# Optimization experiments

Measured on AMD Instinct MI355X. Metric: run time of the kernel, lower is better.

The kernel has to match this reference:

```python
import jax, jax.numpy as jnp
import numpy as np

N, E, IN, HID, OUT, HEADS = 50000, 800000, 256, 256, 128, 4
HC = HID // HEADS  # 64
EPS = 1e-5


def layer_norm(x, g, b):
    mu = x.mean(-1, keepdims=True)
    var = ((x - mu) ** 2).mean(-1, keepdims=True)
    return (x - mu) * jax.lax.rsqrt(var + EPS) * g + b


def gat_conv(x, W, a_s, a_d, bias, src, dst, heads, C, concat):
    # PyG GATConv (eval mode): linear -> per-edge LeakyReLU attention ->
    # segment softmax over destination -> scatter-sum aggregation -> bias
    n = x.shape[0]
    xw = (x @ W).reshape(n, heads, C)                     # [N,H,C]
    al_s = jnp.einsum('nhc,hc->nh', xw, a_s)              # [N,H]
    al_d = jnp.einsum('nhc,hc->nh', xw, a_d)
    e = jax.nn.leaky_relu(al_s[src] + al_d[dst], 0.2)     # [Etot,H]
    m = jax.ops.segment_max(e, dst, num_segments=n)
    ex = jnp.exp(e - m[dst])
    denom = jax.ops.segment_sum(ex, dst, num_segments=n)
    alpha = ex / denom[dst]                               # [Etot,H]
    out = jax.ops.segment_sum(xw[src] * alpha[:, :, None], dst, num_segments=n)
    out = out.reshape(n, heads * C) if concat else out.mean(axis=1)
    return out + bias


def setup_inputs() -> dict:
    key = jax.random.key(0)
    ks = jax.random.split(key, 20)
    s = 0.05
    return {
        'x': jax.random.normal(ks[0], (N, IN), jnp.float32),
        'edge_index': jax.random.randint(ks[1], (2, E), 0, N, jnp.int64),
        'Wp': jax.random.normal(ks[2], (IN, HID), jnp.float32) * s,
        'bp': jnp.zeros((HID,), jnp.float32),
        'W0': jax.random.normal(ks[3], (HID, HEADS * HC), jnp.float32) * s,
        'as0': jax.random.normal(ks[4], (HEADS, HC), jnp.float32) * s,
        'ad0': jax.random.normal(ks[5], (HEADS, HC), jnp.float32) * s,
        'b0': jnp.zeros((HID,), jnp.float32),
        'W1': jax.random.normal(ks[6], (HID, OUT), jnp.float32) * s,
        'as1': jax.random.normal(ks[7], (1, OUT), jnp.float32) * s,
        'ad1': jax.random.normal(ks[8], (1, OUT), jnp.float32) * s,
        'b1': jnp.zeros((OUT,), jnp.float32),
        'g0': jnp.ones((HID,), jnp.float32),
        'be0': jnp.zeros((HID,), jnp.float32),
        'g1': jnp.ones((OUT,), jnp.float32),
        'be1': jnp.zeros((OUT,), jnp.float32),
        'Wo': jax.random.normal(ks[9], (OUT, OUT), jnp.float32) * s,
        'bo': jnp.zeros((OUT,), jnp.float32),
    }


def reference(x, edge_index, Wp, bp, W0, as0, ad0, b0, W1, as1, ad1, b1,
              g0, be0, g1, be1, Wo, bo):
    n = x.shape[0]
    # add self loops (PyG GATConv default)
    ar = jnp.arange(n, dtype=edge_index.dtype)
    src = jnp.concatenate([edge_index[0], ar])
    dst = jnp.concatenate([edge_index[1], ar])

    h = jax.nn.relu(x @ Wp + bp)
    # layer 0: multi-head, concat, LN + residual + relu
    h1 = gat_conv(h, W0, as0, ad0, b0, src, dst, HEADS, HC, True)
    h1 = layer_norm(h1, g0, be0)
    h1 = jax.nn.relu(h1 + h)
    # layer 1: single head, no concat, LN (no residual: shape check still passes
    # only when identity is not None; here identity is None for last layer)
    h2 = gat_conv(h1, W1, as1, ad1, b1, src, dst, 1, OUT, False)
    h2 = layer_norm(h2, g1, be1)
    out = h2 @ Wo + bo
    out = out / jnp.maximum(jnp.linalg.norm(out, axis=-1, keepdims=True), 1e-12)
    return out
```

## Files before the change

kernel.cpp:

```cpp
#include <hip/hip_runtime.h>
#include <hip/hip_bf16.h>

typedef __bf16 bf16x8 __attribute__((ext_vector_type(8)));
typedef __bf16 bf16x4 __attribute__((ext_vector_type(4)));
typedef __bf16 bf16x2 __attribute__((ext_vector_type(2)));
typedef float f32x4 __attribute__((ext_vector_type(4)));

__device__ __forceinline__ float getf(const void* p, size_t i, int isf32){
  return isf32 ? ((const float*)p)[i]
               : __bfloat162float(((const __hip_bfloat16*)p)[i]);
}
__device__ __forceinline__ int getedge(const void* p, long long idx, int is64, int n){
  long long v = is64 ? ((const long long*)p)[idx] : (long long)((const int*)p)[idx];
  v = v < 0 ? 0 : (v >= n ? (long long)(n - 1) : v);
  return (int)v;
}

__device__ __forceinline__ float bfly_sum(float v){
#pragma unroll
  for (int m = 32; m > 0; m >>= 1) v += __shfl_xor(v, m, 64);
  return v;
}

__global__ __launch_bounds__(256) void detect_kernel(const void* x, const void* ei,
                                                     int* flags){
  __shared__ int cnt_sane, cnt_odd;
  int t = threadIdx.x;
  if (t == 0){ cnt_sane = 0; cnt_odd = 0; }
  __syncthreads();
  int sane = 0;
  for (int i = t; i < 4096; i += 256){
    float v = __bfloat162float(((const __hip_bfloat16*)x)[i]);
    if (fabsf(v) < 16.f) sane++;
  }
  atomicAdd(&cnt_sane, sane);
  int odd = 0;
  for (int i = t; i < 512; i += 256){
    if (((const int*)ei)[2 * i + 1] != 0) odd++;
  }
  atomicAdd(&cnt_odd, odd);
  __syncthreads();
  if (t == 0){
    flags[0] = (cnt_sane < 3900) ? 1 : 0;
    flags[1] = (cnt_odd == 0) ? 1 : 0;
  }
}

__global__ __launch_bounds__(256) void count_kernel(const void* __restrict__ ei, long long E,
                                                    int n, const int* __restrict__ flags,
                                                    int* __restrict__ cnt){
  int i = blockIdx.x * blockDim.x + threadIdx.x;
  if (i < E){
    int d = getedge(ei, E + i, flags[1], n);
    atomicAdd(&cnt[d], 1);
  }
}

__global__ __launch_bounds__(1024) void scan_kernel(const int* __restrict__ cnt, int* __restrict__ off,
                                                    int* __restrict__ pos, int n){
  __shared__ int wsum[16];
  __shared__ int carry_s;
  int tid = threadIdx.x, lane = tid & 63, wv = tid >> 6;
  if (tid == 0) carry_s = 0;
  __syncthreads();
  for (int base = 0; base < n; base += 4096){
    int i0 = base + tid * 4;
    int v0 = 0, v1 = 0, v2 = 0, v3 = 0;
    if (i0 + 3 < n){
      int4 q = *(const int4*)(cnt + i0);
      v0 = q.x; v1 = q.y; v2 = q.z; v3 = q.w;
    } else {
      if (i0 < n)     v0 = cnt[i0];
      if (i0 + 1 < n) v1 = cnt[i0 + 1];
      if (i0 + 2 < n) v2 = cnt[i0 + 2];
      if (i0 + 3 < n) v3 = cnt[i0 + 3];
    }
    int s4 = v0 + v1 + v2 + v3;
    int s = s4;
#pragma unroll
    for (int o = 1; o < 64; o <<= 1){ int t = __shfl_up(s, o, 64); if (lane >= o) s += t; }
    if (lane == 63) wsum[wv] = s;
    __syncthreads();
    int wo = 0;
    for (int w = 0; w < wv; w++) wo += wsum[w];
    int carry = carry_s;
    int e0 = carry + wo + s - s4;
    if (i0 + 3 < n){
      int4 o4; o4.x = e0; o4.y = e0 + v0; o4.z = e0 + v0 + v1; o4.w = e0 + v0 + v1 + v2;
      *(int4*)(off + i0) = o4;
      *(int4*)(pos + i0) = o4;
    } else {
      if (i0 < n)     { off[i0] = e0;               pos[i0] = e0; }
      if (i0 + 1 < n) { off[i0+1] = e0+v0;          pos[i0+1] = e0+v0; }
      if (i0 + 2 < n) { off[i0+2] = e0+v0+v1;       pos[i0+2] = e0+v0+v1; }
      if (i0 + 3 < n) { off[i0+3] = e0+v0+v1+v2;    pos[i0+3] = e0+v0+v1+v2; }
    }
    __syncthreads();
    if (tid == 0){
      int tot = 0;
      for (int w = 0; w < 16; w++) tot += wsum[w];
      carry_s = carry + tot;
    }
    __syncthreads();
  }
  if (tid == 0) off[n] = carry_s;
}

__global__ __launch_bounds__(256) void fill_kernel(const void* __restrict__ ei, long long E,
                                                   int n, const int* __restrict__ flags,
                                                   int* __restrict__ pos, int* __restrict__ bsrc){
  int i = blockIdx.x * blockDim.x + threadIdx.x;
  if (i < E){
    int d = getedge(ei, E + i, flags[1], n);
    int s = getedge(ei, i, flags[1], n);
    int p = atomicAdd(&pos[d], 1);
    bsrc[p] = s;
  }
}

__global__ __launch_bounds__(256) void transpose_all_kernel(
    const void* __restrict__ Wp, const void* __restrict__ W0,
    const void* __restrict__ W1, const void* __restrict__ Wo,
    const int* __restrict__ flags,
    __hip_bfloat16* __restrict__ btp, __hip_bfloat16* __restrict__ bt0,
    __hip_bfloat16* __restrict__ bt1, __hip_bfloat16* __restrict__ bto)
{
  int f0 = flags[0];
  int o = blockIdx.x * 256 + threadIdx.x;
  const void* W; __hip_bfloat16* B; int K, N, loc;
  if (o < 65536)       { W = Wp; B = btp; K = 256; N = 256; loc = o; }
  else if (o < 131072) { W = W0; B = bt0; K = 256; N = 256; loc = o - 65536; }
  else if (o < 163840) { W = W1; B = bt1; K = 256; N = 128; loc = o - 131072; }
  else if (o < 180224) { W = Wo; B = bto; K = 128; N = 128; loc = o - 163840; }
  else return;
  int nn = loc / K, kk = loc - nn * K;
  B[loc] = __float2bfloat16(getf(W, (size_t)kk * N + nn, f0));
}

__device__ __forceinline__ bf16x8 pk8(f32x4 u, f32x4 w){
  bf16x8 r;
  r[0] = (__bf16)u.x; r[1] = (__bf16)u.y; r[2] = (__bf16)u.z; r[3] = (__bf16)u.w;
  r[4] = (__bf16)w.x; r[5] = (__bf16)w.y; r[6] = (__bf16)w.z; r[7] = (__bf16)w.w;
  return r;
}

template<int AMODE, bool OUTF, bool OUTB, bool RELU, bool BIAS, bool NORM, int ALMODE>
__global__ __launch_bounds__(256) void gemm_direct_kernel(
    const void* __restrict__ A, const __hip_bfloat16* __restrict__ Bt,
    const void* __restrict__ bias, const void* __restrict__ a_s, const void* __restrict__ a_d,
    const int* __restrict__ flags,
    float* __restrict__ Cf, __hip_bfloat16* __restrict__ Cb,
    float* __restrict__ als, float* __restrict__ ald,
    int M, int N, int K)
{
  const int f0 = flags[0];
  const bool af32 = (AMODE == 1) && (f0 != 0);
  int t = threadIdx.x;
  int wave = t >> 6, lane = t & 63;
  int q = lane >> 4, mi = lane & 15;
  int bm = blockIdx.x * 128 + wave * 32;
  int bn = blockIdx.y * 128;

  int r0 = min(bm + mi, M - 1);
  int r1 = min(bm + 16 + mi, M - 1);

  f32x4 acc[2][8] = {};

  if (af32){
    const float* Af = (const float*)A;
    const float* p0 = Af + (size_t)r0 * K + q * 8;
    const float* p1 = Af + (size_t)r1 * K + q * 8;
#pragma unroll 2
    for (int k0 = 0; k0 < K; k0 += 32){
      f32x4 u0 = *(const f32x4*)(p0 + k0);
      f32x4 w0 = *(const f32x4*)(p0 + k0 + 4);
      f32x4 u1 = *(const f32x4*)(p1 + k0);
      f32x4 w1 = *(const f32x4*)(p1 + k0 + 4);
      bf16x8 a0 = pk8(u0, w0);
      bf16x8 a1 = pk8(u1, w1);
#pragma unroll
      for (int nt = 0; nt < 8; nt++){
        bf16x8 b = *(const bf16x8*)(Bt + (size_t)(bn + nt * 16 + mi) * K + k0 + q * 8);
        acc[0][nt] = __builtin_amdgcn_mfma_f32_16x16x32_bf16(a0, b, acc[0][nt], 0, 0, 0);
        acc[1][nt] = __builtin_amdgcn_mfma_f32_16x16x32_bf16(a1, b, acc[1][nt], 0, 0, 0);
      }
    }
  } else {
    const __hip_bfloat16* Ab = (const __hip_bfloat16*)A;
    const __hip_bfloat16* p0 = Ab + (size_t)r0 * K + q * 8;
    const __hip_bfloat16* p1 = Ab + (size_t)r1 * K + q * 8;
#pragma unroll 2
    for (int k0 = 0; k0 < K; k0 += 32){
      bf16x8 a0 = *(const bf16x8*)(p0 + k0);
      bf16x8 a1 = *(const bf16x8*)(p1 + k0);
#pragma unroll
      for (int nt = 0; nt < 8; nt++){
        bf16x8 b = *(const bf16x8*)(Bt + (size_t)(bn + nt * 16 + mi) * K + k0 + q * 8);
        acc[0][nt] = __builtin_amdgcn_mfma_f32_16x16x32_bf16(a0, b, acc[0][nt], 0, 0, 0);
        acc[1][nt] = __builtin_amdgcn_mfma_f32_16x16x32_bf16(a1, b, acc[1][nt], 0, 0, 0);
      }
    }
  }

  float bv[8], asv[8], adv[8];
  if (BIAS){
#pragma unroll
    for (int nt = 0; nt < 8; nt++) bv[nt] = getf(bias, bn + nt * 16 + mi, f0);
  }
  if (ALMODE != 0){
#pragma unroll
    for (int nt = 0; nt < 8; nt++){
      asv[nt] = getf(a_s, bn + nt * 16 + mi, f0);
      adv[nt] = getf(a_d, bn + nt * 16 + mi, f0);
    }
  }
#pragma unroll
  for (int mt = 0; mt < 2; mt++){
#pragma unroll
    for (int r = 0; r < 4; r++){
      int row = bm + mt * 16 + q * 4 + r;
      float vv[8];
#pragma unroll
      for (int nt = 0; nt < 8; nt++){
        float v = acc[mt][nt][r];
        if (BIAS) v += bv[nt];
        if (RELU) v = fmaxf(v, 0.f);
        vv[nt] = v;
      }
      if (NORM){
        float ss = 0.f;
#pragma unroll
        for (int nt = 0; nt < 8; nt++) ss += vv[nt] * vv[nt];
        ss += __shfl_xor(ss, 1, 64);
        ss += __shfl_xor(ss, 2, 64);
        ss += __shfl_xor(ss, 4, 64);
        ss += __shfl_xor(ss, 8, 64);
        float inv = 1.f / fmaxf(sqrtf(ss), 1e-12f);
#pragma unroll
        for (int nt = 0; nt < 8; nt++) vv[nt] *= inv;
      }
      if (ALMODE == 1){
        float ps0 = 0.f, pd0 = 0.f, ps1 = 0.f, pd1 = 0.f;
#pragma unroll
        for (int nt = 0; nt < 4; nt++){ ps0 += vv[nt] * asv[nt]; pd0 += vv[nt] * adv[nt]; }
#pragma unroll
        for (int nt = 4; nt < 8; nt++){ ps1 += vv[nt] * asv[nt]; pd1 += vv[nt] * adv[nt]; }
#pragma unroll
        for (int m = 1; m < 16; m <<= 1){
          ps0 += __shfl_xor(ps0, m, 64); pd0 += __shfl_xor(pd0, m, 64);
          ps1 += __shfl_xor(ps1, m, 64); pd1 += __shfl_xor(pd1, m, 64);
        }
        if ((lane & 15) == 0 && row < M){
          int h0 = blockIdx.y * 2;
          als[(size_t)row * 4 + h0]     = ps0; ald[(size_t)row * 4 + h0]     = pd0;
          als[(size_t)row * 4 + h0 + 1] = ps1; ald[(size_t)row * 4 + h0 + 1] = pd1;
        }
      } else if (ALMODE == 2){
        float ps = 0.f, pd = 0.f;
#pragma unroll
        for (int nt = 0; nt < 8; nt++){ ps += vv[nt] * asv[nt]; pd += vv[nt] * adv[nt]; }
#pragma unroll
        for (int m = 1; m < 16; m <<= 1){
          ps += __shfl_xor(ps, m, 64); pd += __shfl_xor(pd, m, 64);
        }
        if ((lane & 15) == 0 && row < M){ als[row] = ps; ald[row] = pd; }
      }
      if (row < M){
#pragma unroll
        for (int nt = 0; nt < 8; nt++){
          int col = bn + nt * 16 + mi;
          size_t idx = (size_t)row * N + col;
          if (OUTF) Cf[idx] = vv[nt];
          if (OUTB) Cb[idx] = __float2bfloat16(vv[nt]);
        }
      }
    }
  }
}

#define FMA4(U, W) do { \
  m0 += (W) * __uint_as_float((U).x << 16); \
  m1 += (W) * __uint_as_float((U).x & 0xffff0000u); \
  m2 += (W) * __uint_as_float((U).y << 16); \
  m3 += (W) * __uint_as_float((U).y & 0xffff0000u); \
} while (0)

__global__ __launch_bounds__(256) void gather0_kernel(
    const __hip_bfloat16* __restrict__ xw, const float* __restrict__ als, const float* __restrict__ ald,
    const int* __restrict__ bsrc, const int* __restrict__ off,
    const void* __restrict__ bias, const void* __restrict__ gamma,
    const void* __restrict__ beta, const int* __restrict__ flags,
    __hip_bfloat16* __restrict__ hbuf, int n)
{
  int f0 = flags[0];
  int t = threadIdx.x, wv = t >> 6, lane = t & 63;
  int i = blockIdx.x * 4 + wv;
  if (i >= n) return;
  int head = lane >> 4;
  int ch = lane * 4;
  int e0 = off[i], jend = off[i + 1];

  float m0 = 0.f, m1 = 0.f, m2 = 0.f, m3 = 0.f;

  float aldi = ald[(size_t)i * 4 + head];

  float se = als[(size_t)i * 4 + head] + aldi;
  se = (se > 0.f) ? se : 0.2f * se;
  float eself = __expf(se);
  {
    uint2 u = *(const uint2*)(xw + (size_t)i * 256 + ch);
    FMA4(u, eself);
  }
  float wacc = eself;

  int j = e0;
  for (; j + 3 < jend; j += 4){
    int s0 = bsrc[j], s1 = bsrc[j + 1], s2 = bsrc[j + 2], s3 = bsrc[j + 3];
    float l0 = als[(size_t)s0 * 4 + head] + aldi;
    float l1 = als[(size_t)s1 * 4 + head] + aldi;
    float l2 = als[(size_t)s2 * 4 + head] + aldi;
    float l3 = als[(size_t)s3 * 4 + head] + aldi;
    l0 = (l0 > 0.f) ? l0 : 0.2f * l0;
    l1 = (l1 > 0.f) ? l1 : 0.2f * l1;
    l2 = (l2 > 0.f) ? l2 : 0.2f * l2;
    l3 = (l3 > 0.f) ? l3 : 0.2f * l3;
    float w0 = __expf(l0), w1 = __expf(l1), w2 = __expf(l2), w3 = __expf(l3);
    uint2 U0 = *(const uint2*)(xw + (size_t)s0 * 256 + ch);
    uint2 U1 = *(const uint2*)(xw + (size_t)s1 * 256 + ch);
    uint2 U2 = *(const uint2*)(xw + (size_t)s2 * 256 + ch);
    uint2 U3 = *(const uint2*)(xw + (size_t)s3 * 256 + ch);
    wacc += w0 + w1 + w2 + w3;
    FMA4(U0, w0); FMA4(U1, w1); FMA4(U2, w2); FMA4(U3, w3);
  }
  for (; j < jend; j++){
    int s0 = bsrc[j];
    float l0 = als[(size_t)s0 * 4 + head] + aldi;
    l0 = (l0 > 0.f) ? l0 : 0.2f * l0;
    float w0 = __expf(l0);
    uint2 U0 = *(const uint2*)(xw + (size_t)s0 * 256 + ch);
    wacc += w0;
    FMA4(U0, w0);
  }

  float rl = 1.f / wacc;
  float v0 = m0 * rl + getf(bias, ch + 0, f0);
  float v1 = m1 * rl + getf(bias, ch + 1, f0);
  float v2 = m2 * rl + getf(bias, ch + 2, f0);
  float v3 = m3 * rl + getf(bias, ch + 3, f0);

  float mu = bfly_sum(v0 + v1 + v2 + v3) * (1.f / 256.f);
  float d0 = v0 - mu, d1 = v1 - mu, d2 = v2 - mu, d3 = v3 - mu;
  float var = bfly_sum(d0 * d0 + d1 * d1 + d2 * d2 + d3 * d3) * (1.f / 256.f);
  float rs = rsqrtf(var + 1e-5f);

  bf16x4 rb = *(const bf16x4*)(hbuf + (size_t)i * 256 + ch);
  float y0 = fmaxf(d0 * rs * getf(gamma, ch + 0, f0) + getf(beta, ch + 0, f0) + (float)rb[0], 0.f);
  float y1 = fmaxf(d1 * rs * getf(gamma, ch + 1, f0) + getf(beta, ch + 1, f0) + (float)rb[1], 0.f);
  float y2 = fmaxf(d2 * rs * getf(gamma, ch + 2, f0) + getf(beta, ch + 2, f0) + (float)rb[2], 0.f);
  float y3 = fmaxf(d3 * rs * getf(gamma, ch + 3, f0) + getf(beta, ch + 3, f0) + (float)rb[3], 0.f);

  bf16x4 o;
  o[0] = (__bf16)y0; o[1] = (__bf16)y1; o[2] = (__bf16)y2; o[3] = (__bf16)y3;
  *(bf16x4*)(hbuf + (size_t)i * 256 + ch) = o;
}

#define FMA2(U, W) do { \
  m0 += (W) * __uint_as_float((U) << 16); \
  m1 += (W) * __uint_as_float((U) & 0xffff0000u); \
} while (0)

__global__ __launch_bounds__(256) void gather1_kernel(
    const __hip_bfloat16* __restrict__ xw, const float* __restrict__ als, const float* __restrict__ ald,
    const int* __restrict__ bsrc, const int* __restrict__ off,
    const void* __restrict__ bias, const void* __restrict__ gamma,
    const void* __restrict__ beta, const int* __restrict__ flags,
    __hip_bfloat16* __restrict__ outb, int n)
{
  int f0 = flags[0];
  int t = threadIdx.x, wv = t >> 6, lane = t & 63;
  int i = blockIdx.x * 4 + wv;
  if (i >= n) return;
  int ch = lane * 2;
  int e0 = off[i], jend = off[i + 1];

  float m0 = 0.f, m1 = 0.f;

  float aldi = ald[i];
  float se = als[i] + aldi;
  se = (se > 0.f) ? se : 0.2f * se;
  float eself = __expf(se);
  {
    unsigned u = *(const unsigned*)(xw + (size_t)i * 128 + ch);
    FMA2(u, eself);
  }
  float wacc = eself;

  int j = e0;
  for (; j + 3 < jend; j += 4){
    int s0 = bsrc[j], s1 = bsrc[j + 1], s2 = bsrc[j + 2], s3 = bsrc[j + 3];
    float l0 = als[s0] + aldi, l1 = als[s1] + aldi, l2 = als[s2] + aldi, l3 = als[s3] + aldi;
    l0 = (l0 > 0.f) ? l0 : 0.2f * l0;
    l1 = (l1 > 0.f) ? l1 : 0.2f * l1;
    l2 = (l2 > 0.f) ? l2 : 0.2f * l2;
    l3 = (l3 > 0.f) ? l3 : 0.2f * l3;
    float w0 = __expf(l0), w1 = __expf(l1), w2 = __expf(l2), w3 = __expf(l3);
    unsigned U0 = *(const unsigned*)(xw + (size_t)s0 * 128 + ch);
    unsigned U1 = *(const unsigned*)(xw + (size_t)s1 * 128 + ch);
    unsigned U2 = *(const unsigned*)(xw + (size_t)s2 * 128 + ch);
    unsigned U3 = *(const unsigned*)(xw + (size_t)s3 * 128 + ch);
    wacc += w0 + w1 + w2 + w3;
    FMA2(U0, w0); FMA2(U1, w1); FMA2(U2, w2); FMA2(U3, w3);
  }
  for (; j < jend; j++){
    int s0 = bsrc[j];
    float l0 = als[s0] + aldi;
    l0 = (l0 > 0.f) ? l0 : 0.2f * l0;
    float w0 = __expf(l0);
    unsigned U0 = *(const unsigned*)(xw + (size_t)s0 * 128 + ch);
    wacc += w0;
    FMA2(U0, w0);
  }

  float rl = 1.f / wacc;
  float v0 = m0 * rl + getf(bias, ch + 0, f0);
  float v1 = m1 * rl + getf(bias, ch + 1, f0);

  float mu = bfly_sum(v0 + v1) * (1.f / 128.f);
  float d0 = v0 - mu, d1 = v1 - mu;
  float var = bfly_sum(d0 * d0 + d1 * d1) * (1.f / 128.f);
  float rs = rsqrtf(var + 1e-5f);

  float y0 = d0 * rs * getf(gamma, ch + 0, f0) + getf(beta, ch + 0, f0);
  float y1 = d1 * rs * getf(gamma, ch + 1, f0) + getf(beta, ch + 1, f0);

  bf16x2 o;
  o[0] = (__bf16)y0; o[1] = (__bf16)y1;
  *(bf16x2*)(outb + (size_t)i * 128 + ch) = o;
}

extern "C" void kernel_launch(void* const* d_in, const int* in_sizes, int n_in,
                              void* d_out, int out_size, void* d_ws, size_t ws_size,
                              hipStream_t stream)
{
  const void* x   = d_in[0];
  const void* ei  = d_in[1];
  const void* Wp  = d_in[2];
  const void* bp  = d_in[3];
  const void* W0  = d_in[4];
  const void* as0 = d_in[5];
  const void* ad0 = d_in[6];
  const void* b0  = d_in[7];
  const void* W1  = d_in[8];
  const void* as1 = d_in[9];
  const void* ad1 = d_in[10];
  const void* b1  = d_in[11];
  const void* g0  = d_in[12];
  const void* be0 = d_in[13];
  const void* g1  = d_in[14];
  const void* be1 = d_in[15];
  const void* Wo  = d_in[16];
  const void* bo  = d_in[17];
  float* outp = (float*)d_out;

  const int n = in_sizes[0] / 256;
  const int E = in_sizes[1] / 2;

  char* w = (char*)d_ws;
  size_t SZ = (size_t)n * 256 * sizeof(float);
  __hip_bfloat16* h_bf  = (__hip_bfloat16*)w;
  __hip_bfloat16* xw_bf = (__hip_bfloat16*)(w + SZ / 2);
  char* p = w + SZ;
  int* flags = (int*)p; p += 64;
  float* als0 = (float*)p; p += (size_t)n * 4 * sizeof(float);
  float* ald0 = (float*)p; p += (size_t)n * 4 * sizeof(float);
  float* als1 = (float*)p; p += (size_t)n * sizeof(float);
  float* ald1 = (float*)p; p += (size_t)n * sizeof(float);
  int* cnt  = (int*)p; p += (size_t)n * sizeof(int);
  int* offb = (int*)p; p += (size_t)(n + 4) * sizeof(int);
  int* pos  = (int*)p; p += (size_t)n * sizeof(int);
  int* bsrc = (int*)p; p += (size_t)E * sizeof(int);
  p = (char*)(((uintptr_t)p + 15) & ~(uintptr_t)15);
  __hip_bfloat16* bt_p = (__hip_bfloat16*)p; p += (size_t)256 * 256 * 2;
  __hip_bfloat16* bt_0 = (__hip_bfloat16*)p; p += (size_t)256 * 256 * 2;
  __hip_bfloat16* bt_1 = (__hip_bfloat16*)p; p += (size_t)128 * 256 * 2;
  __hip_bfloat16* bt_o = (__hip_bfloat16*)p; p += (size_t)128 * 128 * 2;

  detect_kernel<<<1, 256, 0, stream>>>(x, ei, flags);

  transpose_all_kernel<<<704, 256, 0, stream>>>(Wp, W0, W1, Wo, flags, bt_p, bt_0, bt_1, bt_o);

  hipMemsetAsync(cnt, 0, (size_t)n * sizeof(int), stream);
  count_kernel<<<(E + 255) / 256, 256, 0, stream>>>(ei, E, n, flags, cnt);
  scan_kernel<<<1, 1024, 0, stream>>>(cnt, offb, pos, n);
  fill_kernel<<<(E + 255) / 256, 256, 0, stream>>>(ei, E, n, flags, pos, bsrc);

  int gm = (n + 127) / 128;
  int gn4 = (n + 3) / 4;

  gemm_direct_kernel<1, false, true, true, true, false, 0><<<dim3(gm, 2), 256, 0, stream>>>(
      x, bt_p, bp, nullptr, nullptr, flags, nullptr, h_bf, nullptr, nullptr, n, 256, 256);
  gemm_direct_kernel<0, false, true, false, false, false, 1><<<dim3(gm, 2), 256, 0, stream>>>(
      h_bf, bt_0, nullptr, as0, ad0, flags, nullptr, xw_bf, als0, ald0, n, 256, 256);
  gather0_kernel<<<gn4, 256, 0, stream>>>(xw_bf, als0, ald0, bsrc, offb, b0, g0, be0,
                                          flags, h_bf, n);
  gemm_direct_kernel<0, false, true, false, false, false, 2><<<dim3(gm, 1), 256, 0, stream>>>(
      h_bf, bt_1, nullptr, as1, ad1, flags, nullptr, xw_bf, als1, ald1, n, 128, 256);
  gather1_kernel<<<gn4, 256, 0, stream>>>(xw_bf, als1, ald1, bsrc, offb, b1, g1, be1,
                                          flags, h_bf, n);
  gemm_direct_kernel<0, true, false, false, true, true, 0><<<dim3(gm, 1), 256, 0, stream>>>(
      h_bf, bt_o, bo, nullptr, nullptr, flags, outp, nullptr, nullptr, nullptr, n, 128, 128);
}
```

Before: 496.4 us.

## Sort nodes by degree and split each wave across two edge streams in gathers

Adds a degree histogram, scan and scatter that build a node order sorted by descending in-degree, so the waves in a block see similar amounts of work. Both gather kernels now split each 64-lane wave into two half-waves that process alternating edges with wider per-lane loads (8 or 4 bf16 channels). The half-wave partial sums are combined with a cross-lane shuffle before the layer norm. This costs three small extra kernels and a loss of node locality in the output writes.

New measurement: 821.7 us. +65.5%, slower.

```diff
diff --git a/kernel.cpp b/kernel.cpp
--- a/kernel.cpp
+++ b/kernel.cpp
@@ -5,6 +5,7 @@
 typedef __bf16 bf16x4 __attribute__((ext_vector_type(4)));
 typedef __bf16 bf16x2 __attribute__((ext_vector_type(2)));
 typedef float f32x4 __attribute__((ext_vector_type(4)));
+typedef unsigned u32x4 __attribute__((ext_vector_type(4)));
 
 __device__ __forceinline__ float getf(const void* p, size_t i, int isf32){
   return isf32 ? ((const float*)p)[i]
@@ -21,6 +22,9 @@
   for (int m = 32; m > 0; m >>= 1) v += __shfl_xor(v, m, 64);
   return v;
 }
+
+__device__ __forceinline__ float bf_lo(unsigned u){ return __uint_as_float(u << 16); }
+__device__ __forceinline__ float bf_hi(unsigned u){ return __uint_as_float(u & 0xffff0000u); }
 
 __global__ __launch_bounds__(256) void detect_kernel(const void* x, const void* ei,
                                                      int* flags){
@@ -118,6 +122,37 @@
   }
 }
 
+__global__ __launch_bounds__(256) void deghist_kernel(const int* __restrict__ cnt, int n,
+                                                      int* __restrict__ hist){
+  int i = blockIdx.x * 256 + threadIdx.x;
+  if (i < n){ int b = min(cnt[i], 255); atomicAdd(&hist[b], 1); }
+}
+
+__global__ __launch_bounds__(256) void degscan_kernel(const int* __restrict__ hist,
+                                                      int* __restrict__ binpos){
+  __shared__ int h[256];
+  int t = threadIdx.x;
+  h[t] = hist[t];
+  __syncthreads();
+  if (t == 0){
+    int acc = 0;
+    for (int b = 255; b >= 0; b--){ int c = h[b]; h[b] = acc; acc += c; }
+  }
+  __syncthreads();
+  binpos[t] = h[t];
+}
+
+__global__ __launch_bounds__(256) void degscatter_kernel(const int* __restrict__ cnt, int n,
+                                                         int* __restrict__ binpos,
+                                                         int* __restrict__ order){
+  int i = blockIdx.x * 256 + threadIdx.x;
+  if (i < n){
+    int b = min(cnt[i], 255);
+    int p = atomicAdd(&binpos[b], 1);
+    order[p] = i;
+  }
+}
+
 __global__ __launch_bounds__(256) void transpose_all_kernel(
     const void* __restrict__ Wp, const void* __restrict__ W0,
     const void* __restrict__ W1, const void* __restrict__ Wo,
@@ -278,44 +313,53 @@
   }
 }
 
-#define FMA4(U, W) do { \
-  m0 += (W) * __uint_as_float((U).x << 16); \
-  m1 += (W) * __uint_as_float((U).x & 0xffff0000u); \
-  m2 += (W) * __uint_as_float((U).y << 16); \
-  m3 += (W) * __uint_as_float((U).y & 0xffff0000u); \
+#define UFMA8(U, W) do { \
+  m0 += (W) * bf_lo((U).x); m1 += (W) * bf_hi((U).x); \
+  m2 += (W) * bf_lo((U).y); m3 += (W) * bf_hi((U).y); \
+  m4 += (W) * bf_lo((U).z); m5 += (W) * bf_hi((U).z); \
+  m6 += (W) * bf_lo((U).w); m7 += (W) * bf_hi((U).w); \
+} while (0)
+
+#define UFMA4(U, W) do { \
+  m0 += (W) * bf_lo((U).x); m1 += (W) * bf_hi((U).x); \
+  m2 += (W) * bf_lo((U).y); m3 += (W) * bf_hi((U).y); \
 } while (0)
 
 __global__ __launch_bounds__(256) void gather0_kernel(
     const __hip_bfloat16* __restrict__ xw, const float* __restrict__ als, const float* __restrict__ ald,
-    const int* __restrict__ bsrc, const int* __restrict__ off,
+    const int* __restrict__ bsrc, const int* __restrict__ off, const int* __restrict__ order,
     const void* __restrict__ bias, const void* __restrict__ gamma,
     const void* __restrict__ beta, const int* __restrict__ flags,
     __hip_bfloat16* __restrict__ hbuf, int n)
 {
   int f0 = flags[0];
   int t = threadIdx.x, wv = t >> 6, lane = t & 63;
-  int i = blockIdx.x * 4 + wv;
-  if (i >= n) return;
-  int head = lane >> 4;
-  int ch = lane * 4;
+  int idx = blockIdx.x * 4 + wv;
+  if (idx >= n) return;
+  int i = order[idx];
+  int es = lane >> 5;
+  int sl = lane & 31;
+  int ch = sl * 8;
+  int head = sl >> 3;
   int e0 = off[i], jend = off[i + 1];
 
-  float m0 = 0.f, m1 = 0.f, m2 = 0.f, m3 = 0.f;
-
+  float m0=0.f,m1=0.f,m2=0.f,m3=0.f,m4=0.f,m5=0.f,m6=0.f,m7=0.f;
   float aldi = ald[(size_t)i * 4 + head];
 
   float se = als[(size_t)i * 4 + head] + aldi;
   se = (se > 0.f) ? se : 0.2f * se;
   float eself = __expf(se);
-  {
-    uint2 u = *(const uint2*)(xw + (size_t)i * 256 + ch);
-    FMA4(u, eself);
-  }
-  float wacc = eself;
-
-  int j = e0;
-  for (; j + 3 < jend; j += 4){
-    int s0 = bsrc[j], s1 = bsrc[j + 1], s2 = bsrc[j + 2], s3 = bsrc[j + 3];
+  float wacc = 0.f;
+  if (es == 0){
+    uint4 u = *(const uint4*)(xw + (size_t)i * 256 + ch);
+    UFMA8(u, eself);
+    wacc = eself;
+  }
+
+  for (int j = e0 + es; j < jend; j += 8){
+    int j1 = j + 2, j2 = j + 4, j3 = j + 6;
+    int c1 = min(j1, jend - 1), c2 = min(j2, jend - 1), c3 = min(j3, jend - 1);
+    int s0 = bsrc[j], s1 = bsrc[c1], s2 = bsrc[c2], s3 = bsrc[c3];
     float l0 = als[(size_t)s0 * 4 + head] + aldi;
     float l1 = als[(size_t)s1 * 4 + head] + aldi;
     float l2 = als[(size_t)s2 * 4 + head] + aldi;
@@ -324,118 +368,130 @@
     l1 = (l1 > 0.f) ? l1 : 0.2f * l1;
     l2 = (l2 > 0.f) ? l2 : 0.2f * l2;
     l3 = (l3 > 0.f) ? l3 : 0.2f * l3;
-    float w0 = __expf(l0), w1 = __expf(l1), w2 = __expf(l2), w3 = __expf(l3);
-    uint2 U0 = *(const uint2*)(xw + (size_t)s0 * 256 + ch);
-    uint2 U1 = *(const uint2*)(xw + (size_t)s1 * 256 + ch);
-    uint2 U2 = *(const uint2*)(xw + (size_t)s2 * 256 + ch);
-    uint2 U3 = *(const uint2*)(xw + (size_t)s3 * 256 + ch);
+    float w0 = __expf(l0);
+    float w1 = (j1 < jend) ? __expf(l1) : 0.f;
+    float w2 = (j2 < jend) ? __expf(l2) : 0.f;
+    float w3 = (j3 < jend) ? __expf(l3) : 0.f;
+    uint4 U0 = *(const uint4*)(xw + (size_t)s0 * 256 + ch);
+    uint4 U1 = *(const uint4*)(xw + (size_t)s1 * 256 + ch);
+    uint4 U2 = *(const uint4*)(xw + (size_t)s2 * 256 + ch);
+    uint4 U3 = *(const uint4*)(xw + (size_t)s3 * 256 + ch);
     wacc += w0 + w1 + w2 + w3;
-    FMA4(U0, w0); FMA4(U1, w1); FMA4(U2, w2); FMA4(U3, w3);
-  }
-  for (; j < jend; j++){
-    int s0 = bsrc[j];
-    float l0 = als[(size_t)s0 * 4 + head] + aldi;
-    l0 = (l0 > 0.f) ? l0 : 0.2f * l0;
-    float w0 = __expf(l0);
-    uint2 U0 = *(const uint2*)(xw + (size_t)s0 * 256 + ch);
-    wacc += w0;
-    FMA4(U0, w0);
-  }
+    UFMA8(U0, w0); UFMA8(U1, w1); UFMA8(U2, w2); UFMA8(U3, w3);
+  }
+
+  m0 += __shfl_xor(m0, 32, 64); m1 += __shfl_xor(m1, 32, 64);
+  m2 += __shfl_xor(m2, 32, 64); m3 += __shfl_xor(m3, 32, 64);
+  m4 += __shfl_xor(m4, 32, 64); m5 += __shfl_xor(m5, 32, 64);
+  m6 += __shfl_xor(m6, 32, 64); m7 += __shfl_xor(m7, 32, 64);
+  wacc += __shfl_xor(wacc, 32, 64);
 
   float rl = 1.f / wacc;
   float v0 = m0 * rl + getf(bias, ch + 0, f0);
   float v1 = m1 * rl + getf(bias, ch + 1, f0);
   float v2 = m2 * rl + getf(bias, ch + 2, f0);
   float v3 = m3 * rl + getf(bias, ch + 3, f0);
-
-  float mu = bfly_sum(v0 + v1 + v2 + v3) * (1.f / 256.f);
-  float d0 = v0 - mu, d1 = v1 - mu, d2 = v2 - mu, d3 = v3 - mu;
-  float var = bfly_sum(d0 * d0 + d1 * d1 + d2 * d2 + d3 * d3) * (1.f / 256.f);
+  float v4 = m4 * rl + getf(bias, ch + 4, f0);
+  float v5 = m5 * rl + getf(bias, ch + 5, f0);
+  float v6 = m6 * rl + getf(bias, ch + 6, f0);
+  float v7 = m7 * rl + getf(bias, ch + 7, f0);
+
+  float mu = bfly_sum(v0+v1+v2+v3+v4+v5+v6+v7) * (1.f / 512.f);
+  float d0=v0-mu,d1=v1-mu,d2=v2-mu,d3=v3-mu,d4=v4-mu,d5=v5-mu,d6=v6-mu,d7=v7-mu;
+  float var = bfly_sum(d0*d0+d1*d1+d2*d2+d3*d3+d4*d4+d5*d5+d6*d6+d7*d7) * (1.f / 512.f);
   float rs = rsqrtf(var + 1e-5f);
 
-  bf16x4 rb = *(const bf16x4*)(hbuf + (size_t)i * 256 + ch);
-  float y0 = fmaxf(d0 * rs * getf(gamma, ch + 0, f0) + getf(beta, ch + 0, f0) + (float)rb[0], 0.f);
-  float y1 = fmaxf(d1 * rs * getf(gamma, ch + 1, f0) + getf(beta, ch + 1, f0) + (float)rb[1], 0.f);
-  float y2 = fmaxf(d2 * rs * getf(gamma, ch + 2, f0) + getf(beta, ch + 2, f0) + (float)rb[2], 0.f);
-  float y3 = fmaxf(d3 * rs * getf(gamma, ch + 3, f0) + getf(beta, ch + 3, f0) + (float)rb[3], 0.f);
-
-  bf16x4 o;
-  o[0] = (__bf16)y0; o[1] = (__bf16)y1; o[2] = (__bf16)y2; o[3] = (__bf16)y3;
-  *(bf16x4*)(hbuf + (size_t)i * 256 + ch) = o;
-}
-
-#define FMA2(U, W) do { \
-  m0 += (W) * __uint_as_float((U) << 16); \
-  m1 += (W) * __uint_as_float((U) & 0xffff0000u); \
-} while (0)
+  if (es == 0){
+    u32x4 rbu = __builtin_nontemporal_load((const u32x4*)(hbuf + (size_t)i * 256 + ch));
+    bf16x8 rb = __builtin_bit_cast(bf16x8, rbu);
+    bf16x8 o;
+    float y;
+    y = d0 * rs * getf(gamma, ch+0, f0) + getf(beta, ch+0, f0) + (float)rb[0]; o[0] = (__bf16)fmaxf(y, 0.f);
+    y = d1 * rs * getf(gamma, ch+1, f0) + getf(beta, ch+1, f0) + (float)rb[1]; o[1] = (__bf16)fmaxf(y, 0.f);
+    y = d2 * rs * getf(gamma, ch+2, f0) + getf(beta, ch+2, f0) + (float)rb[2]; o[2] = (__bf16)fmaxf(y, 0.f);
+    y = d3 * rs * getf(gamma, ch+3, f0) + getf(beta, ch+3, f0) + (float)rb[3]; o[3] = (__bf16)fmaxf(y, 0.f);
+    y = d4 * rs * getf(gamma, ch+4, f0) + getf(beta, ch+4, f0) + (float)rb[4]; o[4] = (__bf16)fmaxf(y, 0.f);
+    y = d5 * rs * getf(gamma, ch+5, f0) + getf(beta, ch+5, f0) + (float)rb[5]; o[5] = (__bf16)fmaxf(y, 0.f);
+    y = d6 * rs * getf(gamma, ch+6, f0) + getf(beta, ch+6, f0) + (float)rb[6]; o[6] = (__bf16)fmaxf(y, 0.f);
+    y = d7 * rs * getf(gamma, ch+7, f0) + getf(beta, ch+7, f0) + (float)rb[7]; o[7] = (__bf16)fmaxf(y, 0.f);
+    *(bf16x8*)(hbuf + (size_t)i * 256 + ch) = o;
+  }
+}
 
 __global__ __launch_bounds__(256) void gather1_kernel(
     const __hip_bfloat16* __restrict__ xw, const float* __restrict__ als, const float* __restrict__ ald,
-    const int* __restrict__ bsrc, const int* __restrict__ off,
+    const int* __restrict__ bsrc, const int* __restrict__ off, const int* __restrict__ order,
     const void* __restrict__ bias, const void* __restrict__ gamma,
     const void* __restrict__ beta, const int* __restrict__ flags,
     __hip_bfloat16* __restrict__ outb, int n)
 {
   int f0 = flags[0];
   int t = threadIdx.x, wv = t >> 6, lane = t & 63;
-  int i = blockIdx.x * 4 + wv;
-  if (i >= n) return;
-  int ch = lane * 2;
+  int idx = blockIdx.x * 4 + wv;
+  if (idx >= n) return;
+  int i = order[idx];
+  int es = lane >> 5;
+  int sl = lane & 31;
+  int ch = sl * 4;
   int e0 = off[i], jend = off[i + 1];
 
-  float m0 = 0.f, m1 = 0.f;
-
+  float m0=0.f,m1=0.f,m2=0.f,m3=0.f;
   float aldi = ald[i];
   float se = als[i] + aldi;
   se = (se > 0.f) ? se : 0.2f * se;
   float eself = __expf(se);
-  {
-    unsigned u = *(const unsigned*)(xw + (size_t)i * 128 + ch);
-    FMA2(u, eself);
-  }
-  float wacc = eself;
-
-  int j = e0;
-  for (; j + 3 < jend; j += 4){
-    int s0 = bsrc[j], s1 = bsrc[j + 1], s2 = bsrc[j + 2], s3 = bsrc[j + 3];
+  float wacc = 0.f;
+  if (es == 0){
+    uint2 u = *(const uint2*)(xw + (size_t)i * 128 + ch);
+    UFMA4(u, eself);
+    wacc = eself;
+  }
+
+  for (int j = e0 + es; j < jend; j += 8){
+    int j1 = j + 2, j2 = j + 4, j3 = j + 6;
+    int c1 = min(j1, jend - 1), c2 = min(j2, jend - 1), c3 = min(j3, jend - 1);
+    int s0 = bsrc[j], s1 = bsrc[c1], s2 = bsrc[c2], s3 = bsrc[c3];
     float l0 = als[s0] + aldi, l1 = als[s1] + aldi, l2 = als[s2] + aldi, l3 = als[s3] + aldi;
     l0 = (l0 > 0.f) ? l0 : 0.2f * l0;
     l1 = (l1 > 0.f) ? l1 : 0.2f * l1;
     l2 = (l2 > 0.f) ? l2 : 0.2f * l2;
     l3 = (l3 > 0.f) ? l3 : 0.2f * l3;
-    float w0 = __expf(l0), w1 = __expf(l1), w2 = __expf(l2), w3 = __expf(l3);
-    unsigned U0 = *(const unsigned*)(xw + (size_t)s0 * 128 + ch);
-    unsigned U1 = *(const unsigned*)(xw + (size_t)s1 * 128 + ch);
-    unsigned U2 = *(const unsigned*)(xw + (size_t)s2 * 128 + ch);
-    unsigned U3 = *(const unsigned*)(xw + (size_t)s3 * 128 + ch);
+    float w0 = __expf(l0);
+    float w1 = (j1 < jend) ? __expf(l1) : 0.f;
+    float w2 = (j2 < jend) ? __expf(l2) : 0.f;
+    float w3 = (j3 < jend) ? __expf(l3) : 0.f;
+    uint2 U0 = *(const uint2*)(xw + (size_t)s0 * 128 + ch);
+    uint2 U1 = *(const uint2*)(xw + (size_t)s1 * 128 + ch);
+    uint2 U2 = *(const uint2*)(xw + (size_t)s2 * 128 + ch);
+    uint2 U3 = *(const uint2*)(xw + (size_t)s3 * 128 + ch);
     wacc += w0 + w1 + w2 + w3;
-    FMA2(U0, w0); FMA2(U1, w1); FMA2(U2, w2); FMA2(U3, w3);
-  }
-  for (; j < jend; j++){
-    int s0 = bsrc[j];
-    float l0 = als[s0] + aldi;
-    l0 = (l0 > 0.f) ? l0 : 0.2f * l0;
-    float w0 = __expf(l0);
-    unsigned U0 = *(const unsigned*)(xw + (size_t)s0 * 128 + ch);
-    wacc += w0;
-    FMA2(U0, w0);
-  }
+    UFMA4(U0, w0); UFMA4(U1, w1); UFMA4(U2, w2); UFMA4(U3, w3);
+  }
+
+  m0 += __shfl_xor(m0, 32, 64); m1 += __shfl_xor(m1, 32, 64);
+  m2 += __shfl_xor(m2, 32, 64); m3 += __shfl_xor(m3, 32, 64);
+  wacc += __shfl_xor(wacc, 32, 64);
 
   float rl = 1.f / wacc;
   float v0 = m0 * rl + getf(bias, ch + 0, f0);
   float v1 = m1 * rl + getf(bias, ch + 1, f0);
-
-  float mu = bfly_sum(v0 + v1) * (1.f / 128.f);
-  float d0 = v0 - mu, d1 = v1 - mu;
-  float var = bfly_sum(d0 * d0 + d1 * d1) * (1.f / 128.f);
+  float v2 = m2 * rl + getf(bias, ch + 2, f0);
+  float v3 = m3 * rl + getf(bias, ch + 3, f0);
+
+  float mu = bfly_sum(v0 + v1 + v2 + v3) * (1.f / 256.f);
+  float d0 = v0 - mu, d1 = v1 - mu, d2 = v2 - mu, d3 = v3 - mu;
+  float var = bfly_sum(d0*d0 + d1*d1 + d2*d2 + d3*d3) * (1.f / 256.f);
   float rs = rsqrtf(var + 1e-5f);
 
-  float y0 = d0 * rs * getf(gamma, ch + 0, f0) + getf(beta, ch + 0, f0);
-  float y1 = d1 * rs * getf(gamma, ch + 1, f0) + getf(beta, ch + 1, f0);
-
-  bf16x2 o;
-  o[0] = (__bf16)y0; o[1] = (__bf16)y1;
-  *(bf16x2*)(outb + (size_t)i * 128 + ch) = o;
+  if (es == 0){
+    bf16x4 o;
+    float y;
+    y = d0 * rs * getf(gamma, ch+0, f0) + getf(beta, ch+0, f0); o[0] = (__bf16)y;
+    y = d1 * rs * getf(gamma, ch+1, f0) + getf(beta, ch+1, f0); o[1] = (__bf16)y;
+    y = d2 * rs * getf(gamma, ch+2, f0) + getf(beta, ch+2, f0); o[2] = (__bf16)y;
+    y = d3 * rs * getf(gamma, ch+3, f0) + getf(beta, ch+3, f0); o[3] = (__bf16)y;
+    *(bf16x4*)(outb + (size_t)i * 128 + ch) = o;
+  }
 }
 
 extern "C" void kernel_launch(void* const* d_in, const int* in_sizes, int n_in,
@@ -475,10 +531,13 @@
   float* ald0 = (float*)p; p += (size_t)n * 4 * sizeof(float);
   float* als1 = (float*)p; p += (size_t)n * sizeof(float);
   float* ald1 = (float*)p; p += (size_t)n * sizeof(float);
-  int* cnt  = (int*)p; p += (size_t)n * sizeof(int);
-  int* offb = (int*)p; p += (size_t)(n + 4) * sizeof(int);
-  int* pos  = (int*)p; p += (size_t)n * sizeof(int);
-  int* bsrc = (int*)p; p += (size_t)E * sizeof(int);
+  int* cnt    = (int*)p; p += (size_t)n * sizeof(int);
+  int* hist   = (int*)p; p += 256 * sizeof(int);
+  int* binpos = (int*)p; p += 256 * sizeof(int);
+  int* order  = (int*)p; p += (size_t)n * sizeof(int);
+  int* offb   = (int*)p; p += (size_t)(n + 4) * sizeof(int);
+  int* pos    = (int*)p; p += (size_t)n * sizeof(int);
+  int* bsrc   = (int*)p; p += (size_t)E * sizeof(int);
   p = (char*)(((uintptr_t)p + 15) & ~(uintptr_t)15);
   __hip_bfloat16* bt_p = (__hip_bfloat16*)p; p += (size_t)256 * 256 * 2;
   __hip_bfloat16* bt_0 = (__hip_bfloat16*)p; p += (size_t)256 * 256 * 2;
@@ -489,9 +548,13 @@
 
   transpose_all_kernel<<<704, 256, 0, stream>>>(Wp, W0, W1, Wo, flags, bt_p, bt_0, bt_1, bt_o);
 
-  hipMemsetAsync(cnt, 0, (size_t)n * sizeof(int), stream);
+  (void)hipMemsetAsync(cnt, 0, ((size_t)n + 256) * sizeof(int), stream);
   count_kernel<<<(E + 255) / 256, 256, 0, stream>>>(ei, E, n, flags, cnt);
   scan_kernel<<<1, 1024, 0, stream>>>(cnt, offb, pos, n);
+  int gnn = (n + 255) / 256;
+  deghist_kernel<<<gnn, 256, 0, stream>>>(cnt, n, hist);
+  degscan_kernel<<<1, 256, 0, stream>>>(hist, binpos);
+  degscatter_kernel<<<gnn, 256, 0, stream>>>(cnt, n, binpos, order);
   fill_kernel<<<(E + 255) / 256, 256, 0, stream>>>(ei, E, n, flags, pos, bsrc);
 
   int gm = (n + 127) / 128;
@@ -501,11 +564,11 @@
       x, bt_p, bp, nullptr, nullptr, flags, nullptr, h_bf, nullptr, nullptr, n, 256, 256);
   gemm_direct_kernel<0, false, true, false, false, false, 1><<<dim3(gm, 2), 256, 0, stream>>>(
       h_bf, bt_0, nullptr, as0, ad0, flags, nullptr, xw_bf, als0, ald0, n, 256, 256);
-  gather0_kernel<<<gn4, 256, 0, stream>>>(xw_bf, als0, ald0, bsrc, offb, b0, g0, be0,
+  gather0_kernel<<<gn4, 256, 0, stream>>>(xw_bf, als0, ald0, bsrc, offb, order, b0, g0, be0,
                                           flags, h_bf, n);
   gemm_direct_kernel<0, false, true, false, false, false, 2><<<dim3(gm, 1), 256, 0, stream>>>(
       h_bf, bt_1, nullptr, as1, ad1, flags, nullptr, xw_bf, als1, ald1, n, 128, 256);
-  gather1_kernel<<<gn4, 256, 0, stream>>>(xw_bf, als1, ald1, bsrc, offb, b1, g1, be1,
+  gather1_kernel<<<gn4, 256, 0, stream>>>(xw_bf, als1, ald1, bsrc, offb, order, b1, g1, be1,
                                           flags, h_bf, n);
   gemm_direct_kernel<0, true, false, false, true, true, 0><<<dim3(gm, 1), 256, 0, stream>>>(
       h_bf, bt_o, bo, nullptr, nullptr, flags, outp, nullptr, nullptr, nullptr, n, 128, 128);
```
